# Kernel optimization log

Hardware: AMD Instinct MI355X
Metric: run time of the kernel (lower is better)

## Reference

```python
import jax, jax.numpy as jnp
import numpy as np

B, C, H, W = 4, 256, 64, 64
RC = 32  # reduced channels = C // reduction


def setup_inputs() -> dict:
    key = jax.random.key(0)
    ks = jax.random.split(key, 5)
    return {
        "x": jax.random.normal(ks[0], (B, C, H, W), dtype=jnp.float32),
        "context": jax.random.normal(ks[1], (B, C, H, W), dtype=jnp.float32),
        "Wq": jax.random.normal(ks[2], (RC, C), dtype=jnp.float32) * 0.02,
        "bq": jnp.zeros((RC,), dtype=jnp.float32),
        "Wk": jax.random.normal(ks[3], (RC, C), dtype=jnp.float32) * 0.02,
        "bk": jnp.zeros((RC,), dtype=jnp.float32),
        "Wv": jax.random.normal(ks[4], (C, C), dtype=jnp.float32) * 0.02,
        "bv": jnp.zeros((C,), dtype=jnp.float32),
        "gamma": jnp.ones((1,), dtype=jnp.float32),
    }


def reference(x, context, Wq, bq, Wk, bk, Wv, bv, gamma):
    b, c, h, w = x.shape
    _, _, hc, wc = context.shape
    n, m = h * w, hc * wc
    xf = x.reshape(b, c, n)          # (B,C,N)
    cf = context.reshape(b, c, m)    # (B,C,M)
    # 1x1 conv projections == per-pixel linear
    q = jnp.einsum('rc,bcn->bnr', Wq, xf) + bq            # (B,N,RC)
    k = jnp.einsum('rc,bcm->brm', Wk, cf) + bk[:, None]   # (B,RC,M)
    v = jnp.einsum('dc,bcm->bdm', Wv, cf) + bv[:, None]   # (B,C,M)
    scale = 1.0 / jnp.sqrt(jnp.asarray(q.shape[-1], dtype=q.dtype))
    attn = jax.nn.softmax(jnp.einsum('bnr,brm->bnm', q, k) * scale, axis=-1)  # (B,N,M)
    out = jnp.einsum('bdm,bnm->bdn', v, attn).reshape(b, c, h, w)
    return gamma * out + x
```

## Files before the change

kernel.cpp:

```cpp
#include <hip/hip_runtime.h>
#include <hip/hip_bf16.h>


#define B_ 4
#define C_ 256
#define N_ 4096
#define M_ 4096
#define SCALE_ 0.17677669529663687f

typedef __bf16 bf16x8 __attribute__((ext_vector_type(8)));
typedef float f32x4 __attribute__((ext_vector_type(4)));
typedef float f32x16 __attribute__((ext_vector_type(16)));
typedef int i32x8 __attribute__((ext_vector_type(8)));

#define AS1 __attribute__((address_space(1)))
#define AS3 __attribute__((address_space(3)))

static __device__ __forceinline__ unsigned short f2bf(float f) {
    unsigned int u = __float_as_uint(f);
    return (unsigned short)((u + 0x7fffu + ((u >> 16) & 1u)) >> 16);
}
static __device__ __forceinline__ unsigned bfpk(float a, float b) {
    return (unsigned)f2bf(a) | ((unsigned)f2bf(b) << 16);
}
static __device__ __forceinline__ void p_barrier() {
    asm volatile("s_waitcnt lgkmcnt(0)" ::: "memory");
    __builtin_amdgcn_s_barrier();
    asm volatile("" ::: "memory");
}

__global__ __launch_bounds__(256) void prep(
        const float* __restrict__ Wq, const float* __restrict__ Wk,
        const float* __restrict__ Wv, uint4* __restrict__ Wqf,
        uint4* __restrict__ Wkf, uint4* __restrict__ Wvf) {
    int bid = blockIdx.x, t = threadIdx.x;
    const float* W;
    uint4* dst;
    int frag;
    if (bid < 32)      { W = Wv; dst = Wvf; frag = (bid * 256 + t) >> 6; }
    else if (bid < 36) { W = Wq; dst = Wqf; frag = ((bid - 32) * 256 + t) >> 6; }
    else               { W = Wk; dst = Wkf; frag = ((bid - 36) * 256 + t) >> 6; }
    int lane = t & 63, low = lane & 15, q = lane >> 4;
    int fch = frag & 7, fr = frag >> 3;
    const float* wp = W + (size_t)(fr * 16 + low) * C_ + fch * 32 + q * 8;
    float4 w0 = *(const float4*)wp;
    float4 w1 = *(const float4*)(wp + 4);
    uint4 pk = {bfpk(w0.x, w0.y), bfpk(w0.z, w0.w),
                bfpk(w1.x, w1.y), bfpk(w1.z, w1.w)};
    dst[(size_t)frag * 64 + lane] = pk;
}

__global__ __launch_bounds__(256, 2) void fused_proj(
        const float* __restrict__ x, const float* __restrict__ ctx,
        const uint4* __restrict__ Wqf, const uint4* __restrict__ Wkf,
        const uint4* __restrict__ Wvf,
        const float* __restrict__ bq, const float* __restrict__ bk,
        const float* __restrict__ bv,
        unsigned short* __restrict__ Qf, unsigned short* __restrict__ Kf,
        unsigned char* __restrict__ Vf) {
    __shared__ unsigned short X[64][264];
    __shared__ unsigned short Pl[4][16 * 40];
    __shared__ unsigned char  Vw[4][16 * 40];

    int bid = blockIdx.x;
    bool isX = bid >= 256;
    int lb = bid & 255;
    int b = lb >> 6, pt64 = lb & 63;
    const float* __restrict__ in = (isX ? x : ctx) + (size_t)b * C_ * N_ + pt64 * 64;
    int t = threadIdx.x, wg = t >> 6, lane = t & 63;
    int low = lane & 15, q = lane >> 4;

    {
        int pL = lane;
        const float* s0 = in + pL;
#pragma unroll
        for (int ct = 0; ct < 4; ct++) {
            const float* s2 = s0 + (size_t)(ct * 64 + wg * 16) * N_;
            float v[16];
#pragma unroll
            for (int k = 0; k < 16; k++) v[k] = s2[(size_t)k * N_];
#pragma unroll
            for (int k = 0; k < 16; k += 2)
                *(unsigned*)&X[pL][ct * 64 + wg * 16 + k] = bfpk(v[k], v[k + 1]);
        }
    }
    __syncthreads();

    {
        const uint4* __restrict__ Wf = isX ? Wqf : Wkf;
        const float* __restrict__ bias = isX ? bq : bk;
        unsigned short* __restrict__ dst = isX ? Qf : Kf;
        bf16x8 xf[8];
#pragma unroll
        for (int ch = 0; ch < 8; ch++)
            xf[ch] = *(const bf16x8*)&X[wg * 16 + low][ch * 32 + q * 8];
        const f32x4 zero = {0.f, 0.f, 0.f, 0.f};
        f32x4 acc[2] = {zero, zero};
#pragma unroll
        for (int rt = 0; rt < 2; rt++)
#pragma unroll
            for (int ch = 0; ch < 8; ch++) {
                uint4 wv = Wf[(rt * 8 + ch) * 64 + lane];
                acc[rt] = __builtin_amdgcn_mfma_f32_16x16x32_bf16(
                    __builtin_bit_cast(bf16x8, wv), xf[ch], acc[rt], 0, 0, 0);
            }
        unsigned short* Pw = &Pl[wg][0];
#pragma unroll
        for (int rt = 0; rt < 2; rt++) {
            float b0 = bias[rt * 16 + q * 4 + 0], b1 = bias[rt * 16 + q * 4 + 1];
            float b2 = bias[rt * 16 + q * 4 + 2], b3 = bias[rt * 16 + q * 4 + 3];
            uint2 pk = {bfpk(acc[rt][0] + b0, acc[rt][1] + b1),
                        bfpk(acc[rt][2] + b2, acc[rt][3] + b3)};
            *(uint2*)(Pw + low * 40 + rt * 16 + q * 4) = pk;
        }
        uint4 frag = *(const uint4*)(Pw + low * 40 + q * 8);
        ((uint4*)dst)[((size_t)b * 256 + pt64 * 4 + wg) * 64 + lane] = frag;
    }

    if (!isX) {
        int mstep = wg >> 1, dh = wg & 1;
        bf16x8 vfr[2][8];
#pragma unroll
        for (int mt = 0; mt < 2; mt++)
#pragma unroll
            for (int ch = 0; ch < 8; ch++)
                vfr[mt][ch] = *(const bf16x8*)&X[mstep * 32 + mt * 16 + low][ch * 32 + q * 8];
        unsigned char* Vv = &Vw[wg][0];
        int msg = pt64 * 2 + mstep;
        const f32x4 zero = {0.f, 0.f, 0.f, 0.f};
#pragma unroll
        for (int dt8 = 0; dt8 < 8; dt8++) {
            int dt = dh * 8 + dt8;
            f32x4 a0 = zero, a1 = zero;
#pragma unroll
            for (int ch = 0; ch < 8; ch++) {
                uint4 wv = Wvf[(dt * 8 + ch) * 64 + lane];
                bf16x8 wfr = __builtin_bit_cast(bf16x8, wv);
                a0 = __builtin_amdgcn_mfma_f32_16x16x32_bf16(vfr[0][ch], wfr, a0, 0, 0, 0);
                a1 = __builtin_amdgcn_mfma_f32_16x16x32_bf16(vfr[1][ch], wfr, a1, 0, 0, 0);
            }
            float bb = bv[dt * 16 + low];
            unsigned w0 = __builtin_amdgcn_cvt_pk_fp8_f32(a0[0] + bb, a0[1] + bb, 0, false);
            w0 = __builtin_amdgcn_cvt_pk_fp8_f32(a0[2] + bb, a0[3] + bb, w0, true);
            unsigned w1 = __builtin_amdgcn_cvt_pk_fp8_f32(a1[0] + bb, a1[1] + bb, 0, false);
            w1 = __builtin_amdgcn_cvt_pk_fp8_f32(a1[2] + bb, a1[3] + bb, w1, true);
            *(unsigned*)(Vv + low * 40 + q * 4) = w0;
            *(unsigned*)(Vv + low * 40 + 16 + q * 4) = w1;
            uint2 fr = *(const uint2*)(Vv + low * 40 + q * 8);
            ((uint2*)Vf)[(((size_t)b * 128 + msg) * 16 + dt) * 64 + lane] = fr;
        }
    }
}

__global__ __launch_bounds__(512, 4) void attn(
        const unsigned short* __restrict__ Qf, const unsigned short* __restrict__ Kf,
        const unsigned char* __restrict__ Vf, const float* __restrict__ x,
        const float* __restrict__ gamma, float* __restrict__ out) {
    __shared__ __align__(16) unsigned char Pb[2][2][16 * 80];
    __shared__ float l_sh[2][32];
    __shared__ unsigned Ot[32 * 129];

    int bid = blockIdx.x;
    int xcd = bid & 7;
    int b = xcd >> 1;
    int g = ((xcd & 1) << 6) | (bid >> 3);

    int wave = threadIdx.x >> 6, lane = threadIdx.x & 63;
    int q = lane >> 4, low = lane & 15;
    int hi = lane >> 5;
    int dsel = q & 1;
    int l31 = lane & 31;
    bool isQK = wave < 4;
    int t = wave & 1;
    int h = (wave >> 1) & 1;

    const uint4* Qp = (const uint4*)Qf;
    const uint4* Kp = (const uint4*)Kf + (size_t)b * 256 * 64;
    const uint2* Vq = (const uint2*)(Vf + (size_t)b * 1048576) + (size_t)hi * 1024 + low;
    int dt = wave * 2 + dsel;

    bf16x8 qa;
    if (isQK)
        qa = __builtin_bit_cast(bf16x8, Qp[(size_t)(b * 256 + g * 2 + t) * 64 + lane]);

    f32x16 acc = (f32x16)(0.f);
    float lacc = 0.f;
    const f32x4 zero = {0.f, 0.f, 0.f, 0.f};

    uint4 kv[2];
    f32x4 s[2];
    if (isQK) {
#pragma unroll
        for (int u = 0; u < 2; u++)
            kv[u] = Kp[(size_t)(h * 2 + u) * 64 + lane];
#pragma unroll
        for (int u = 0; u < 2; u++)
            s[u] = __builtin_amdgcn_mfma_f32_16x16x32_bf16(
                __builtin_bit_cast(bf16x8, kv[u]), qa, zero, 0, 0, 0);
#pragma unroll
        for (int u = 0; u < 2; u++)
            kv[u] = Kp[(size_t)(4 + h * 2 + u) * 64 + lane];
        unsigned char* Pw = &Pb[0][t][0];
#pragma unroll
        for (int u = 0; u < 2; u++) {
            float p0 = __expf(s[u][0] * SCALE_), p1 = __expf(s[u][1] * SCALE_);
            float p2 = __expf(s[u][2] * SCALE_), p3 = __expf(s[u][3] * SCALE_);
            lacc += p0 + p1 + p2 + p3;
            unsigned w = __builtin_amdgcn_cvt_pk_fp8_f32(p0, p1, 0, false);
            w = __builtin_amdgcn_cvt_pk_fp8_f32(p2, p3, w, true);
            *(unsigned*)(Pw + low * 80 + h * 32 + u * 16 + q * 4) = w;
        }
    }
    i32x8 vfc;
    {
        const uint2* Vs = Vq + (size_t)dt * 64;
        long* dqw = (long*)&vfc;
#pragma unroll
        for (int ss = 0; ss < 4; ss++)
            dqw[ss] = *(const long*)(Vs + ss * 16);
    }
    p_barrier();

    for (int i = 0; i < 64; i++) {
        int cur = i & 1, nxt = cur ^ 1;
        bool haveNext = (i + 1 < 64);

        i32x8 vfn;
        if (haveNext) {
            const uint2* Vs = Vq + (size_t)(i + 1) * 2048 + dt * 64;
            long* dqw = (long*)&vfn;
#pragma unroll
            for (int ss = 0; ss < 4; ss++)
                dqw[ss] = *(const long*)(Vs + ss * 16);
        }

        if (isQK && haveNext) {
#pragma unroll
            for (int u = 0; u < 2; u++)
                s[u] = __builtin_amdgcn_mfma_f32_16x16x32_bf16(
                    __builtin_bit_cast(bf16x8, kv[u]), qa, zero, 0, 0, 0);
            if (i + 2 < 64) {
#pragma unroll
                for (int u = 0; u < 2; u++)
                    kv[u] = Kp[(size_t)((i + 2) * 4 + h * 2 + u) * 64 + lane];
            }
        }

        {
            const unsigned char* pr = &Pb[cur][0][0] + dsel * 1280 + low * 80 + hi * 32;
            i32x8 pf;
            ((uint4*)&pf)[0] = *(const uint4*)pr;
            ((uint4*)&pf)[1] = *(const uint4*)(pr + 16);
            __builtin_amdgcn_s_setprio(1);
            acc = __builtin_amdgcn_mfma_scale_f32_32x32x64_f8f6f4(
                vfc, pf, acc, 0, 0, 0, 127, 0, 127);
            __builtin_amdgcn_s_setprio(0);
        }

        if (isQK && haveNext) {
            unsigned char* Pw = &Pb[nxt][t][0];
#pragma unroll
            for (int u = 0; u < 2; u++) {
                float p0 = __expf(s[u][0] * SCALE_), p1 = __expf(s[u][1] * SCALE_);
                float p2 = __expf(s[u][2] * SCALE_), p3 = __expf(s[u][3] * SCALE_);
                lacc += p0 + p1 + p2 + p3;
                unsigned w = __builtin_amdgcn_cvt_pk_fp8_f32(p0, p1, 0, false);
                w = __builtin_amdgcn_cvt_pk_fp8_f32(p2, p3, w, true);
                *(unsigned*)(Pw + low * 80 + h * 32 + u * 16 + q * 4) = w;
            }
        }
        if (haveNext) vfc = vfn;
        p_barrier();
    }

    if (isQK) {
        lacc += __shfl_xor(lacc, 16, 64);
        lacc += __shfl_xor(lacc, 32, 64);
        if (lane < 16)
            l_sh[h][t * 16 + low] = lacc;
    }

#pragma unroll
    for (int r = 0; r < 16; r += 2) {
        int col16 = wave * 16 + ((r >> 1) & 1) + 4 * (r >> 2) + 2 * hi;
        Ot[l31 * 129 + col16] = bfpk(acc[r], acc[r + 1]);
    }
    __syncthreads();

    {
        float gm = gamma[0];
        float rinv = gm / (l_sh[0][l31] + l_sh[1][l31]);
        int dh = lane >> 5;
        size_t nb = ((size_t)(b * 256 + wave * 32 + dh * 16)) * 4096
                    + (size_t)g * 32 + l31;
#pragma unroll 4
        for (int j = 0; j < 16; j++) {
            unsigned pk = Ot[l31 * 129 + wave * 16 + dh * 8 + (j >> 1)];
            unsigned bits = (j & 1) ? (pk & 0xffff0000u) : (pk << 16);
            float o = __uint_as_float(bits);
            size_t idx = nb + (size_t)j * 4096;
            out[idx] = o * rinv + x[idx];
        }
    }
}

extern "C" void kernel_launch(void* const* d_in, const int* in_sizes, int n_in,
                              void* d_out, int out_size, void* d_ws, size_t ws_size,
                              hipStream_t stream) {
    const float* x     = (const float*)d_in[0];
    const float* ctx   = (const float*)d_in[1];
    const float* Wq    = (const float*)d_in[2];
    const float* bq    = (const float*)d_in[3];
    const float* Wk    = (const float*)d_in[4];
    const float* bk    = (const float*)d_in[5];
    const float* Wv    = (const float*)d_in[6];
    const float* bv    = (const float*)d_in[7];
    const float* gamma = (const float*)d_in[8];
    float* out = (float*)d_out;

    unsigned short* Qf = (unsigned short*)d_ws;
    unsigned short* Kf = Qf + (size_t)B_ * N_ * 32;
    unsigned char*  Vf = (unsigned char*)(Kf + (size_t)B_ * M_ * 32);
    uint4* Wqf = (uint4*)(Vf + (size_t)B_ * M_ * C_);
    uint4* Wkf = Wqf + 16 * 64;
    uint4* Wvf = Wkf + 16 * 64;

    prep<<<40, 256, 0, stream>>>(Wq, Wk, Wv, Wqf, Wkf, Wvf);
    fused_proj<<<512, 256, 0, stream>>>(x, ctx, Wqf, Wkf, Wvf, bq, bk, bv, Qf, Kf, Vf);
    attn<<<512, 512, 0, stream>>>(Qf, Kf, Vf, x, gamma, out);
}
```

Baseline: 142.2 us.

## Split key range across two wave groups, each computing all PV tiles

```diff
diff --git a/kernel.cpp b/kernel.cpp
--- a/kernel.cpp
+++ b/kernel.cpp
@@ -156,51 +156,54 @@
         const unsigned short* __restrict__ Qf, const unsigned short* __restrict__ Kf,
         const unsigned char* __restrict__ Vf, const float* __restrict__ x,
         const float* __restrict__ gamma, float* __restrict__ out) {
-    __shared__ __align__(16) unsigned char Pb[2][2][16 * 80];
-    __shared__ float l_sh[2][32];
+    __shared__ __align__(16) unsigned char Pb[2][2][2 * 16 * 80];
+    __shared__ float l_sh[4][32];
+    __shared__ unsigned Obuf[32 * 129];
     __shared__ unsigned Ot[32 * 129];
 
     int bid = blockIdx.x;
     int xcd = bid & 7;
     int b = xcd >> 1;
-    int g = ((xcd & 1) << 6) | (bid >> 3);
+    int ng = ((xcd & 1) << 6) | (bid >> 3);
 
     int wave = threadIdx.x >> 6, lane = threadIdx.x & 63;
+    int g = wave >> 2, wg = wave & 3;
     int q = lane >> 4, low = lane & 15;
     int hi = lane >> 5;
     int dsel = q & 1;
     int l31 = lane & 31;
-    bool isQK = wave < 4;
-    int t = wave & 1;
-    int h = (wave >> 1) & 1;
+    int t = wg & 1;
+    int h = wg >> 1;
 
     const uint4* Qp = (const uint4*)Qf;
     const uint4* Kp = (const uint4*)Kf + (size_t)b * 256 * 64;
     const uint2* Vq = (const uint2*)(Vf + (size_t)b * 1048576) + (size_t)hi * 1024 + low;
-    int dt = wave * 2 + dsel;
-
-    bf16x8 qa;
-    if (isQK)
-        qa = __builtin_bit_cast(bf16x8, Qp[(size_t)(b * 256 + g * 2 + t) * 64 + lane]);
-
-    f32x16 acc = (f32x16)(0.f);
+    int slab0 = g * 32;
+
+    bf16x8 qa = __builtin_bit_cast(bf16x8, Qp[(size_t)(b * 256 + ng * 2 + t) * 64 + lane]);
+
+    f32x16 acc2[2];
+    acc2[0] = (f32x16)(0.f);
+    acc2[1] = (f32x16)(0.f);
     float lacc = 0.f;
     const f32x4 zero = {0.f, 0.f, 0.f, 0.f};
 
+    unsigned char* PbG = &Pb[g][0][0];
+
     uint4 kv[2];
     f32x4 s[2];
-    if (isQK) {
+    {
 #pragma unroll
         for (int u = 0; u < 2; u++)
-            kv[u] = Kp[(size_t)(h * 2 + u) * 64 + lane];
+            kv[u] = Kp[(size_t)(slab0 * 4 + h * 2 + u) * 64 + lane];
 #pragma unroll
         for (int u = 0; u < 2; u++)
             s[u] = __builtin_amdgcn_mfma_f32_16x16x32_bf16(
                 __builtin_bit_cast(bf16x8, kv[u]), qa, zero, 0, 0, 0);
 #pragma unroll
         for (int u = 0; u < 2; u++)
-            kv[u] = Kp[(size_t)(4 + h * 2 + u) * 64 + lane];
-        unsigned char* Pw = &Pb[0][t][0];
+            kv[u] = Kp[(size_t)((slab0 + 1) * 4 + h * 2 + u) * 64 + lane];
+        unsigned char* Pw = PbG;
 #pragma unroll
         for (int u = 0; u < 2; u++) {
             float p0 = __expf(s[u][0] * SCALE_), p1 = __expf(s[u][1] * SCALE_);
@@ -208,57 +211,62 @@
             lacc += p0 + p1 + p2 + p3;
             unsigned w = __builtin_amdgcn_cvt_pk_fp8_f32(p0, p1, 0, false);
             w = __builtin_amdgcn_cvt_pk_fp8_f32(p2, p3, w, true);
-            *(unsigned*)(Pw + low * 80 + h * 32 + u * 16 + q * 4) = w;
-        }
-    }
-    i32x8 vfc;
-    {
-        const uint2* Vs = Vq + (size_t)dt * 64;
-        long* dqw = (long*)&vfc;
+            *(unsigned*)(Pw + t * 1280 + low * 80 + h * 32 + u * 16 + q * 4) = w;
+        }
+    }
+    i32x8 vf[2];
+#pragma unroll
+    for (int dg = 0; dg < 2; dg++) {
+        int dt = wg * 4 + dg * 2 + dsel;
+        const uint2* Vs = Vq + (size_t)slab0 * 2048 + dt * 64;
+        long* dqw = (long*)&vf[dg];
 #pragma unroll
         for (int ss = 0; ss < 4; ss++)
             dqw[ss] = *(const long*)(Vs + ss * 16);
     }
     p_barrier();
 
-    for (int i = 0; i < 64; i++) {
+    for (int i = 0; i < 32; i++) {
         int cur = i & 1, nxt = cur ^ 1;
-        bool haveNext = (i + 1 < 64);
-
-        i32x8 vfn;
-        if (haveNext) {
-            const uint2* Vs = Vq + (size_t)(i + 1) * 2048 + dt * 64;
-            long* dqw = (long*)&vfn;
-#pragma unroll
-            for (int ss = 0; ss < 4; ss++)
-                dqw[ss] = *(const long*)(Vs + ss * 16);
-        }
-
-        if (isQK && haveNext) {
+        bool hn = (i + 1 < 32);
+
+        if (hn) {
 #pragma unroll
             for (int u = 0; u < 2; u++)
                 s[u] = __builtin_amdgcn_mfma_f32_16x16x32_bf16(
                     __builtin_bit_cast(bf16x8, kv[u]), qa, zero, 0, 0, 0);
-            if (i + 2 < 64) {
+            if (i + 2 < 32) {
 #pragma unroll
                 for (int u = 0; u < 2; u++)
-                    kv[u] = Kp[(size_t)((i + 2) * 4 + h * 2 + u) * 64 + lane];
+                    kv[u] = Kp[(size_t)((slab0 + i + 2) * 4 + h * 2 + u) * 64 + lane];
             }
         }
 
         {
-            const unsigned char* pr = &Pb[cur][0][0] + dsel * 1280 + low * 80 + hi * 32;
+            const unsigned char* pr = PbG + cur * 2560 + dsel * 1280 + low * 80 + hi * 32;
             i32x8 pf;
             ((uint4*)&pf)[0] = *(const uint4*)pr;
             ((uint4*)&pf)[1] = *(const uint4*)(pr + 16);
-            __builtin_amdgcn_s_setprio(1);
-            acc = __builtin_amdgcn_mfma_scale_f32_32x32x64_f8f6f4(
-                vfc, pf, acc, 0, 0, 0, 127, 0, 127);
-            __builtin_amdgcn_s_setprio(0);
-        }
-
-        if (isQK && haveNext) {
-            unsigned char* Pw = &Pb[nxt][t][0];
+#pragma unroll
+            for (int dg = 0; dg < 2; dg++)
+                acc2[dg] = __builtin_amdgcn_mfma_scale_f32_32x32x64_f8f6f4(
+                    vf[dg], pf, acc2[dg], 0, 0, 0, 127, 0, 127);
+        }
+
+        if (hn) {
+#pragma unroll
+            for (int dg = 0; dg < 2; dg++) {
+                int dt = wg * 4 + dg * 2 + dsel;
+                const uint2* Vs = Vq + (size_t)(slab0 + i + 1) * 2048 + dt * 64;
+                long* dqw = (long*)&vf[dg];
+#pragma unroll
+                for (int ss = 0; ss < 4; ss++)
+                    dqw[ss] = *(const long*)(Vs + ss * 16);
+            }
+        }
+
+        if (hn) {
+            unsigned char* Pw = PbG + nxt * 2560;
 #pragma unroll
             for (int u = 0; u < 2; u++) {
                 float p0 = __expf(s[u][0] * SCALE_), p1 = __expf(s[u][1] * SCALE_);
@@ -266,33 +274,47 @@
                 lacc += p0 + p1 + p2 + p3;
                 unsigned w = __builtin_amdgcn_cvt_pk_fp8_f32(p0, p1, 0, false);
                 w = __builtin_amdgcn_cvt_pk_fp8_f32(p2, p3, w, true);
-                *(unsigned*)(Pw + low * 80 + h * 32 + u * 16 + q * 4) = w;
-            }
-        }
-        if (haveNext) vfc = vfn;
+                *(unsigned*)(Pw + t * 1280 + low * 80 + h * 32 + u * 16 + q * 4) = w;
+            }
+        }
         p_barrier();
     }
 
-    if (isQK) {
-        lacc += __shfl_xor(lacc, 16, 64);
-        lacc += __shfl_xor(lacc, 32, 64);
-        if (lane < 16)
-            l_sh[h][t * 16 + low] = lacc;
-    }
-
-#pragma unroll
-    for (int r = 0; r < 16; r += 2) {
-        int col16 = wave * 16 + ((r >> 1) & 1) + 4 * (r >> 2) + 2 * hi;
-        Ot[l31 * 129 + col16] = bfpk(acc[r], acc[r + 1]);
+    lacc += __shfl_xor(lacc, 16, 64);
+    lacc += __shfl_xor(lacc, 32, 64);
+    if (lane < 16)
+        l_sh[g * 2 + h][t * 16 + low] = lacc;
+
+    if (g == 1) {
+#pragma unroll
+        for (int dg = 0; dg < 2; dg++)
+#pragma unroll
+            for (int k = 0; k < 8; k++) {
+                int col16 = wg * 32 + dg * 16 + (k & 1) + 4 * (k >> 1) + 2 * hi;
+                Obuf[l31 * 129 + col16] = bfpk(acc2[dg][2 * k], acc2[dg][2 * k + 1]);
+            }
+    }
+    __syncthreads();
+    if (g == 0) {
+#pragma unroll
+        for (int dg = 0; dg < 2; dg++)
+#pragma unroll
+            for (int k = 0; k < 8; k++) {
+                int col16 = wg * 32 + dg * 16 + (k & 1) + 4 * (k >> 1) + 2 * hi;
+                unsigned pk = Obuf[l31 * 129 + col16];
+                float a = acc2[dg][2 * k]     + __uint_as_float(pk << 16);
+                float c = acc2[dg][2 * k + 1] + __uint_as_float(pk & 0xffff0000u);
+                Ot[l31 * 129 + col16] = bfpk(a, c);
+            }
     }
     __syncthreads();
 
     {
         float gm = gamma[0];
-        float rinv = gm / (l_sh[0][l31] + l_sh[1][l31]);
-        int dh = lane >> 5;
+        float rinv = gm / (l_sh[0][l31] + l_sh[1][l31] + l_sh[2][l31] + l_sh[3][l31]);
+        int dh = hi;
         size_t nb = ((size_t)(b * 256 + wave * 32 + dh * 16)) * 4096
-                    + (size_t)g * 32 + l31;
+                    + (size_t)ng * 32 + l31;
 #pragma unroll 4
         for (int j = 0; j < 16; j++) {
             unsigned pk = Ot[l31 * 129 + wave * 16 + dh * 8 + (j >> 1)];
```

Result: no change. 144.3 us (+1.5%).
